# Kernel tuning notes

Hardware: AMD Instinct MI355X
Metric: run time of the kernel (lower is better)

## Reference

```python
import jax, jax.numpy as jnp
import numpy as np

P = 7          # pooled output size
SR = 2         # sampling_ratio
S = P * SR     # samples per spatial dim
SCALES = (0.25, 0.125, 0.0625, 0.03125)
K_MIN = 2      # -log2(scales[0])
K_MAX = 5      # -log2(scales[-1])
CANON_S0 = 224.0
CANON_LVL = 4.0
EPS = 1e-6
IMG = 800.0


def _roi_align(feat, rois, scale):
    """ROIAlign (aligned=False, caffe2/maskrcnn-benchmark semantics).
    feat: [B,C,H,W]; rois: [N,5] = (batch_idx, x1,y1,x2,y2) in image coords.
    Returns [N,C,P,P]."""
    B, C, H, W = feat.shape
    N = rois.shape[0]
    bidx = rois[:, 0].astype(jnp.int32)
    x1 = rois[:, 1] * scale
    y1 = rois[:, 2] * scale
    x2 = rois[:, 3] * scale
    y2 = rois[:, 4] * scale
    rw = jnp.maximum(x2 - x1, 1.0)
    rh = jnp.maximum(y2 - y1, 1.0)
    bw = rw / P
    bh = rh / P
    # per-bin sub-sample offsets: (bin + (i+0.5)/SR) for i in 0..SR-1 -> [S]
    grid = (jnp.arange(P, dtype=feat.dtype)[:, None]
            + (jnp.arange(SR, dtype=feat.dtype)[None, :] + 0.5) / SR).reshape(-1)
    ys = y1[:, None] + grid[None, :] * bh[:, None]   # [N,S]
    xs = x1[:, None] + grid[None, :] * bw[:, None]   # [N,S]

    def prep(c, L):
        valid = (c > -1.0) & (c < L)
        c = jnp.clip(c, 0.0, L - 1.0)
        lo = jnp.minimum(jnp.floor(c).astype(jnp.int32), L - 2)
        return valid, lo, c - lo

    vy, y0, fy = prep(ys, H)
    vx, x0, fx = prep(xs, W)

    flat = feat.transpose(0, 2, 3, 1).reshape(B * H * W, C)  # [BHW,C]
    base = bidx[:, None, None] * (H * W)
    idx00 = base + y0[:, :, None] * W + x0[:, None, :]       # [N,S,S]
    hy = (1.0 - fy)[:, :, None]
    ly = fy[:, :, None]
    hx = (1.0 - fx)[:, None, :]
    lx = fx[:, None, :]
    val = ((hy * hx)[..., None] * flat[idx00]
           + (hy * lx)[..., None] * flat[idx00 + 1]
           + (ly * hx)[..., None] * flat[idx00 + W]
           + (ly * lx)[..., None] * flat[idx00 + W + 1])     # [N,S,S,C]
    mask = (vy[:, :, None] & vx[:, None, :])[..., None]
    val = jnp.where(mask, val, 0.0)
    # average SRxSR sub-samples per bin
    out = val.reshape(N, P, SR, P, SR, C).mean(axis=(2, 4))  # [N,P,P,C]
    return out.transpose(0, 3, 1, 2)                         # [N,C,P,P]


def _map_levels(boxes):
    # LevelMapper heuristic (FPN paper); area in original image coords.
    area = (boxes[:, 2] - boxes[:, 0]) * (boxes[:, 3] - boxes[:, 1])
    s = jnp.sqrt(area)
    lvl = jnp.floor(CANON_LVL + jnp.log2(s / CANON_S0 + EPS))
    lvl = jnp.clip(lvl, K_MIN, K_MAX)
    return lvl.astype(jnp.int32) - K_MIN


def setup_inputs() -> dict:
    key = jax.random.key(0)
    k1, k2, k3, k4 = jax.random.split(key, 4)
    N = 512
    cx = jax.random.uniform(k1, (N,)) * IMG
    cy = jax.random.uniform(k2, (N,)) * IMG
    # log-uniform box sizes in [16, 512] px -> spans all FPN levels
    sz = 2.0 ** (jax.random.uniform(k3, (N, 2)) * 5.0 + 4.0)
    x1 = jnp.clip(cx - sz[:, 0] * 0.5, 0.0, IMG - 2.0)
    y1 = jnp.clip(cy - sz[:, 1] * 0.5, 0.0, IMG - 2.0)
    x2 = jnp.clip(cx + sz[:, 0] * 0.5, x1 + 1.0, IMG)
    y2 = jnp.clip(cy + sz[:, 1] * 0.5, y1 + 1.0, IMG)
    boxes = jnp.stack([x1, y1, x2, y2], axis=1).astype(jnp.float32)
    batch_ids = jnp.sort(jax.random.randint(k4, (N,), 0, 2)).astype(jnp.int64)
    fk = jax.random.split(jax.random.key(1), 4)
    feats = {
        f"feat{i}": jax.random.normal(fk[i], (2, 256, 200 // (2 ** i), 200 // (2 ** i)),
                                      dtype=jnp.float32)
        for i in range(4)
    }
    return dict(boxes=boxes, batch_ids=batch_ids, **feats)


def reference(feat0, feat1, feat2, feat3, boxes, batch_ids):
    feats = (feat0, feat1, feat2, feat3)
    rois = jnp.concatenate([batch_ids.astype(boxes.dtype)[:, None], boxes], axis=1)
    levels = _map_levels(boxes)                      # [N] in 0..3
    result = jnp.zeros((boxes.shape[0], feat0.shape[1], P, P), dtype=feat0.dtype)
    for lvl in range(len(feats)):
        pooled = _roi_align(feats[lvl], rois, SCALES[lvl])
        result = jnp.where(levels[:, None, None, None] == lvl, pooled, result)
    return result
```

## Files before the change

### kernel.cpp

```cpp
#include <hip/hip_runtime.h>

#define P 7
#define NCH 256
#define NPP 49
#define CHIT 4
#define LDS_CAP 1280

typedef float f2 __attribute__((ext_vector_type(2), aligned(4)));

__device__ __forceinline__ int rfl(int x) { return __builtin_amdgcn_readfirstlane(x); }

__global__ __launch_bounds__(256) void pooler_kernel(
    const float* __restrict__ boxes,
    const int* __restrict__ batch_ids,
    const float* __restrict__ g0, const float* __restrict__ g1,
    const float* __restrict__ g2, const float* __restrict__ g3,
    float* __restrict__ out)
{
    __shared__ float sreg[4][LDS_CAP];

    const int n    = blockIdx.y;
    const int cq   = blockIdx.x;
    const int lane = threadIdx.x;
    const int wy   = threadIdx.y;

    const float x1i = boxes[n*4+0], y1i = boxes[n*4+1];
    const float x2i = boxes[n*4+2], y2i = boxes[n*4+3];
    const float area = (x2i - x1i) * (y2i - y1i);
    float lvlf = floorf(4.0f + log2f(sqrtf(area) / 224.0f + 1e-6f));
    lvlf = fminf(fmaxf(lvlf, 2.0f), 5.0f);
    const int lvl = rfl((int)lvlf - 2);

    const float* feat = (lvl==0) ? g0 : (lvl==1) ? g1 : (lvl==2) ? g2 : g3;
    const int    L    = (lvl==0) ? 200 : (lvl==1) ? 100 : (lvl==2) ? 50 : 25;
    const float scale = (lvl==0) ? 0.25f : (lvl==1) ? 0.125f
                      : (lvl==2) ? 0.0625f : 0.03125f;
    const int b  = batch_ids[n];
    const int LL = L * L;

    const float x1 = x1i * scale, y1 = y1i * scale;
    const float bw = fmaxf(x2i*scale - x1, 1.0f) * (1.0f/7.0f);
    const float bh = fmaxf(y2i*scale - y1, 1.0f) * (1.0f/7.0f);
    const float Lf = (float)L, Lm1 = Lf - 1.0f;
    const int   Lm2 = L - 2;

    const int rx0 = rfl(min((int)fminf(fmaxf(x1 + 0.25f*bw, 0.0f), Lm1), Lm2));
    const int rx1 = rfl(min((int)fminf(fmaxf(x1 + 6.75f*bw, 0.0f), Lm1), Lm2));
    const int ry0 = rfl(min((int)fminf(fmaxf(y1 + 0.25f*bh, 0.0f), Lm1), Lm2));
    const int ry1 = rfl(min((int)fminf(fmaxf(y1 + 6.75f*bh, 0.0f), Lm1), Lm2));
    const int Wr  = rx1 - rx0 + 2;
    const int Hr  = ry1 - ry0 + 2;
    const int stride = Wr | 1;
    const int Hm1 = Hr - 1;
    const int Wc  = Wr - 2;

    const int py = (lane < NPP) ? lane / P : 6;
    const int px = (lane < NPP) ? lane - py * P : 6;
    float wta[2][2], wtb[2][2], wtc[2][2], wtd[2][2];
    int   adr[2][2];
    {
        int   y0[2], x0[2];
        float fy[2], hy[2], vy[2], fx[2], hx[2], vx[2];
#pragma unroll
        for (int s = 0; s < 2; ++s) {
            const float yc = y1 + ((float)py + (s ? 0.75f : 0.25f)) * bh;
            vy[s] = (yc > -1.0f && yc < Lf) ? 1.0f : 0.0f;
            const float ycc = fminf(fmaxf(yc, 0.0f), Lm1);
            y0[s] = min((int)ycc, Lm2);
            fy[s] = ycc - (float)y0[s];
            hy[s] = 1.0f - fy[s];

            const float xc = x1 + ((float)px + (s ? 0.75f : 0.25f)) * bw;
            vx[s] = (xc > -1.0f && xc < Lf) ? 1.0f : 0.0f;
            const float xcc = fminf(fmaxf(xc, 0.0f), Lm1);
            x0[s] = min((int)xcc, Lm2);
            fx[s] = xcc - (float)x0[s];
            hx[s] = 1.0f - fx[s];
        }
#pragma unroll
        for (int sy = 0; sy < 2; ++sy)
#pragma unroll
        for (int sx = 0; sx < 2; ++sx) {
            const float w = 0.25f * vy[sy] * vx[sx];
            wta[sy][sx] = w * hy[sy] * hx[sx];
            wtb[sy][sx] = w * hy[sy] * fx[sx];
            wtc[sy][sx] = w * fy[sy] * hx[sx];
            wtd[sy][sx] = w * fy[sy] * fx[sx];
            adr[sy][sx] = (y0[sy] - ry0) * stride - rx0 + x0[sx];
        }
    }

    const int cw0 = lane << 1;
    const int sub  = lane >> 4;
    const int ccn  = min((lane & 15) << 1, Wc);
    const int gofs = sub * L + ccn;
    const int lofs = sub * stride + ccn;

    float* sp = sreg[wy];
    const int c_first = cq * (CHIT * 4) + wy;
    size_t ob = ((size_t)n * NCH + c_first) * NPP + lane;

    for (int it = 0; it < CHIT; ++it) {
        const int c    = c_first + (it << 2);
        const int poff = rfl((b * NCH + c) * LL + ry0 * L + rx0);
        const float* gp = feat + poff;

        if (Wr > 32) {
            for (int cb = 0; cb < Wr; cb += 128) {
                const int ccc = min(cb + cw0, Wc);
                for (int r = 0; r < Hr; r += 4) {
                    int rr[4]; f2 v[4];
#pragma unroll
                    for (int j = 0; j < 4; ++j) rr[j] = min(r + j, Hm1);
#pragma unroll
                    for (int j = 0; j < 4; ++j)
                        v[j] = *(const f2*)(gp + rr[j] * L + ccc);
#pragma unroll
                    for (int j = 0; j < 4; ++j) {
                        const int a = rr[j] * stride + ccc;
                        sp[a] = v[j].x; sp[a + 1] = v[j].y;
                    }
                }
            }
        } else {
            int r = 0;
            for (; r + 8 <= Hr; r += 8) {
                const f2 vA = *(const f2*)(gp + r * L + gofs);
                const f2 vB = *(const f2*)(gp + (r + 4) * L + gofs);
                const int aA = r * stride + lofs;
                const int aB = (r + 4) * stride + lofs;
                sp[aA] = vA.x; sp[aA + 1] = vA.y;
                sp[aB] = vB.x; sp[aB + 1] = vB.y;
            }
            for (; r < Hr; r += 4) {
                if (sub < Hr - r) {
                    const f2 v = *(const f2*)(gp + r * L + gofs);
                    const int a = r * stride + lofs;
                    sp[a] = v.x; sp[a + 1] = v.y;
                }
            }
        }

        if (lane < NPP) {
            float acc = 0.0f;
#pragma unroll
            for (int sy = 0; sy < 2; ++sy)
#pragma unroll
            for (int sx = 0; sx < 2; ++sx) {
                const int a = adr[sy][sx];
                acc += wta[sy][sx] * sp[a]
                     + wtb[sy][sx] * sp[a + 1]
                     + wtc[sy][sx] * sp[a + stride]
                     + wtd[sy][sx] * sp[a + stride + 1];
            }
            out[ob] = acc;
        }
        ob += (size_t)4 * NPP;
    }
}

extern "C" void kernel_launch(void* const* d_in, const int* in_sizes, int n_in,
                              void* d_out, int out_size, void* d_ws, size_t ws_size,
                              hipStream_t stream) {
    const float* boxes     = (const float*)d_in[0];
    const int*   batch_ids = (const int*)d_in[1];
    const float* g0        = (const float*)d_in[2];
    const float* g1        = (const float*)d_in[3];
    const float* g2        = (const float*)d_in[4];
    const float* g3        = (const float*)d_in[5];
    float* out = (float*)d_out;

    const int N = in_sizes[0] / 4;
    dim3 block(64, 4);
    dim3 grid(NCH / (CHIT * 4), N);
    pooler_kernel<<<grid, block, 0, stream>>>(boxes, batch_ids, g0, g1, g2, g3, out);
}
```

Baseline: 57.49 us.

## Align ROI staging to enable 16-byte vector loads and LDS stores per level

Aligns the staged ROI window's start column to a multiple of 4 (levels 0-1) or 2 (level 2), pads the LDS row stride to avoid bank alignment, and replaces the row-copy loops with level-specialized float4/float2/scalar loads. Each lane is mapped to a power-of-two column slot so several rows are copied per wave pass. This aims to cut the number of global load and LDS store instructions. It enlarges the LDS buffer and may fetch a few extra columns, and the copy loops for small windows now use clamped duplicate rows.

```diff
diff --git a/kernel.cpp b/kernel.cpp
--- a/kernel.cpp
+++ b/kernel.cpp
@@ -4,9 +4,10 @@
 #define NCH 256
 #define NPP 49
 #define CHIT 4
-#define LDS_CAP 1280
+#define LDS_CAP 2048
 
-typedef float f2 __attribute__((ext_vector_type(2), aligned(4)));
+typedef float f2 __attribute__((ext_vector_type(2), aligned(8)));
+typedef float f4 __attribute__((ext_vector_type(4), aligned(16)));
 
 __device__ __forceinline__ int rfl(int x) { return __builtin_amdgcn_readfirstlane(x); }
 
@@ -17,7 +18,7 @@
     const float* __restrict__ g2, const float* __restrict__ g3,
     float* __restrict__ out)
 {
-    __shared__ float sreg[4][LDS_CAP];
+    __shared__ __align__(16) float sreg[4][LDS_CAP];
 
     const int n    = blockIdx.y;
     const int cq   = blockIdx.x;
@@ -48,11 +49,23 @@
     const int rx1 = rfl(min((int)fminf(fmaxf(x1 + 6.75f*bw, 0.0f), Lm1), Lm2));
     const int ry0 = rfl(min((int)fminf(fmaxf(y1 + 0.25f*bh, 0.0f), Lm1), Lm2));
     const int ry1 = rfl(min((int)fminf(fmaxf(y1 + 6.75f*bh, 0.0f), Lm1), Lm2));
-    const int Wr  = rx1 - rx0 + 2;
     const int Hr  = ry1 - ry0 + 2;
-    const int stride = Wr | 1;
     const int Hm1 = Hr - 1;
-    const int Wc  = Wr - 2;
+
+    int rx0a, WrA, stride;
+    if (lvl <= 1) {
+        rx0a = rx0 & ~3;
+        WrA  = (rx1 + 2 - rx0a + 3) & ~3;
+        stride = WrA + 4; if ((stride & 31) == 0) stride += 4;
+    } else if (lvl == 2) {
+        rx0a = rx0 & ~1;
+        WrA  = (rx1 + 2 - rx0a + 1) & ~1;
+        stride = WrA + 2; if ((stride & 31) == 0) stride += 2;
+    } else {
+        rx0a = rx0;
+        WrA  = rx1 + 2 - rx0;
+        stride = WrA | 1;
+    }
 
     const int py = (lane < NPP) ? lane / P : 6;
     const int px = (lane < NPP) ? lane - py * P : 6;
@@ -86,15 +99,24 @@
             wtb[sy][sx] = w * hy[sy] * fx[sx];
             wtc[sy][sx] = w * fy[sy] * hx[sx];
             wtd[sy][sx] = w * fy[sy] * fx[sx];
-            adr[sy][sx] = (y0[sy] - ry0) * stride - rx0 + x0[sx];
+            adr[sy][sx] = (y0[sy] - ry0) * stride - rx0a + x0[sx];
         }
     }
 
-    const int cw0 = lane << 1;
-    const int sub  = lane >> 4;
-    const int ccn  = min((lane & 15) << 1, Wc);
-    const int gofs = sub * L + ccn;
-    const int lofs = sub * stride + ccn;
+    const int qpr  = WrA >> 2;
+    const int p2q  = (qpr > 1) ? (32 - __clz(qpr - 1)) : 0;
+    const int rp4  = 64 >> p2q;
+    const int sub4 = lane >> p2q;
+    const int cq4  = min((lane & ((1 << p2q) - 1)) << 2, WrA - 4);
+    const int ppr  = WrA >> 1;
+    const int p2p  = (ppr > 1) ? (32 - __clz(ppr - 1)) : 0;
+    const int rp2  = 64 >> p2p;
+    const int sub2 = lane >> p2p;
+    const int cp2  = min((lane & ((1 << p2p) - 1)) << 1, WrA - 2);
+    const int p2c  = (WrA > 1) ? (32 - __clz(WrA - 1)) : 0;
+    const int rp1  = 64 >> p2c;
+    const int sub1 = lane >> p2c;
+    const int cc1  = min(lane & ((1 << p2c) - 1), WrA - 1);
 
     float* sp = sreg[wy];
     const int c_first = cq * (CHIT * 4) + wy;
@@ -102,42 +124,35 @@
 
     for (int it = 0; it < CHIT; ++it) {
         const int c    = c_first + (it << 2);
-        const int poff = rfl((b * NCH + c) * LL + ry0 * L + rx0);
+        const int poff = rfl((b * NCH + c) * LL + ry0 * L + rx0a);
         const float* gp = feat + poff;
 
-        if (Wr > 32) {
-            for (int cb = 0; cb < Wr; cb += 128) {
-                const int ccc = min(cb + cw0, Wc);
-                for (int r = 0; r < Hr; r += 4) {
-                    int rr[4]; f2 v[4];
-#pragma unroll
-                    for (int j = 0; j < 4; ++j) rr[j] = min(r + j, Hm1);
-#pragma unroll
-                    for (int j = 0; j < 4; ++j)
-                        v[j] = *(const f2*)(gp + rr[j] * L + ccc);
-#pragma unroll
-                    for (int j = 0; j < 4; ++j) {
-                        const int a = rr[j] * stride + ccc;
-                        sp[a] = v[j].x; sp[a + 1] = v[j].y;
-                    }
-                }
+        if (lvl <= 1) {
+            for (int r = 0; r < Hr; r += 2 * rp4) {
+                const int rA = min(r + sub4, Hm1);
+                const int rB = min(r + rp4 + sub4, Hm1);
+                const f4 vA = *(const f4*)(gp + rA * L + cq4);
+                const f4 vB = *(const f4*)(gp + rB * L + cq4);
+                *(f4*)(sp + rA * stride + cq4) = vA;
+                *(f4*)(sp + rB * stride + cq4) = vB;
+            }
+        } else if (lvl == 2) {
+            for (int r = 0; r < Hr; r += 2 * rp2) {
+                const int rA = min(r + sub2, Hm1);
+                const int rB = min(r + rp2 + sub2, Hm1);
+                const f2 vA = *(const f2*)(gp + rA * L + cp2);
+                const f2 vB = *(const f2*)(gp + rB * L + cp2);
+                *(f2*)(sp + rA * stride + cp2) = vA;
+                *(f2*)(sp + rB * stride + cp2) = vB;
             }
         } else {
-            int r = 0;
-            for (; r + 8 <= Hr; r += 8) {
-                const f2 vA = *(const f2*)(gp + r * L + gofs);
-                const f2 vB = *(const f2*)(gp + (r + 4) * L + gofs);
-                const int aA = r * stride + lofs;
-                const int aB = (r + 4) * stride + lofs;
-                sp[aA] = vA.x; sp[aA + 1] = vA.y;
-                sp[aB] = vB.x; sp[aB + 1] = vB.y;
-            }
-            for (; r < Hr; r += 4) {
-                if (sub < Hr - r) {
-                    const f2 v = *(const f2*)(gp + r * L + gofs);
-                    const int a = r * stride + lofs;
-                    sp[a] = v.x; sp[a + 1] = v.y;
-                }
+            for (int r = 0; r < Hr; r += 2 * rp1) {
+                const int rA = min(r + sub1, Hm1);
+                const int rB = min(r + rp1 + sub1, Hm1);
+                const float vA = gp[rA * L + cc1];
+                const float vB = gp[rB * L + cc1];
+                sp[rA * stride + cc1] = vA;
+                sp[rB * stride + cc1] = vB;
             }
         }
 
```

Result: faster. 52.67 us (-8.4%).
